# Performance work log

Hardware: AMD Instinct MI355X
Metric: run time of the kernel (lower is better)

## Reference

```python
import jax, jax.numpy as jnp
import numpy as np

B, S, D, H, HD, K, FF, G, E = 2, 2048, 512, 8, 64, 31, 2048, 4, 2
EPS = 1e-6


def _layer_norm(x, scale, bias):
    m = jnp.mean(x, axis=-1, keepdims=True)
    v = jnp.var(x, axis=-1, keepdims=True)
    return (x - m) * jax.lax.rsqrt(v + EPS) * scale + bias


def _forward(x, group_ids, p):
    (ln1_s, ln1_b, ck, cb, ln2_s, ln2_b,
     wq, bq, wk, bk, wv, bv, wo, bo, w1, b1, w2, b2) = p
    # ---- conv sublayer: LN -> Conv1d(SAME) -> gelu -> residual ----
    r = x
    h = _layer_norm(x, ln1_s, ln1_b)
    h = jax.lax.conv_general_dilated(h, ck, (1,), 'SAME',
                                     dimension_numbers=('NWC', 'WIO', 'NWC')) + cb
    x = jax.nn.gelu(h) + r
    # ---- self-attention sublayer: LN -> MHA -> residual ----
    r = x
    h = _layer_norm(x, ln2_s, ln2_b)
    q = jnp.einsum('bsd,dhk->bshk', h, wq) + bq   # [B,S,H,HD]
    k = jnp.einsum('bsd,dhk->bshk', h, wk) + bk
    v = jnp.einsum('bsd,dhk->bshk', h, wv) + bv
    scale = jnp.asarray(1.0 / np.sqrt(HD), h.dtype)
    att = jax.nn.softmax(jnp.einsum('bqhk,bshk->bhqs', q, k) * scale, axis=-1)
    o = jnp.einsum('bhqs,bshk->bqhk', att, v)
    x = jnp.einsum('bqhk,hkd->bqd', o, wo) + bo + r
    # ---- MoE sublayer: group tokens -> per-group experts -> mean -> combine ----
    r = x
    xf = x.reshape(-1, D)            # [N, D]
    gid = group_ids.reshape(-1)      # [N]
    # Each token routed by group_id gets the mean over that group's E experts.
    hid = jax.nn.gelu(jnp.einsum('nd,gedf->genf', xf, w1) + b1[:, :, None, :])  # [G,E,N,FF]
    ye = jnp.einsum('genf,gefd->gend', hid, w2) + b2[:, :, None, :]             # [G,E,N,D]
    yg = ye.mean(axis=1)                                                        # [G,N,D]
    sel = yg[gid, jnp.arange(gid.shape[0])]                                     # [N,D] combine by group id
    return sel.reshape(B, S, D) + r


def setup_inputs() -> dict:
    key = jax.random.key(0)
    ks = jax.random.split(key, 12)
    std = 0.02
    f32 = jnp.float32
    return {
        'x': jax.random.normal(ks[0], (B, S, D), f32),
        'group_ids': jax.random.randint(ks[1], (B, S), 0, G, jnp.int32),
        'ln1_scale': jnp.ones((D,), f32), 'ln1_bias': jnp.zeros((D,), f32),
        'conv_kernel': jax.random.normal(ks[2], (K, D, D), f32) * std,
        'conv_bias': jnp.zeros((D,), f32),
        'ln2_scale': jnp.ones((D,), f32), 'ln2_bias': jnp.zeros((D,), f32),
        'wq': jax.random.normal(ks[3], (D, H, HD), f32) * std, 'bq': jnp.zeros((H, HD), f32),
        'wk': jax.random.normal(ks[4], (D, H, HD), f32) * std, 'bk': jnp.zeros((H, HD), f32),
        'wv': jax.random.normal(ks[5], (D, H, HD), f32) * std, 'bv': jnp.zeros((H, HD), f32),
        'wo': jax.random.normal(ks[6], (H, HD, D), f32) * std, 'bo': jnp.zeros((D,), f32),
        'w1': jax.random.normal(ks[7], (G, E, D, FF), f32) * std, 'b1': jnp.zeros((G, E, FF), f32),
        'w2': jax.random.normal(ks[8], (G, E, FF, D), f32) * std, 'b2': jnp.zeros((G, E, D), f32),
    }


def reference(x, group_ids, ln1_scale, ln1_bias, conv_kernel, conv_bias,
              ln2_scale, ln2_bias, wq, bq, wk, bk, wv, bv, wo, bo,
              w1, b1, w2, b2):
    p = (ln1_scale, ln1_bias, conv_kernel, conv_bias, ln2_scale, ln2_bias,
         wq, bq, wk, bk, wv, bv, wo, bo, w1, b1, w2, b2)
    return _forward(x, group_ids, p)
```

## Files before the change

### kernel.cpp

```cpp
#include <hip/hip_runtime.h>
#include <hip/hip_bf16.h>
#include <math.h>
#include <stdint.h>

namespace {

constexpr int B_ = 2, S_ = 2048, D_ = 512, H_ = 8, HD_ = 64, K_ = 31,
              FF_ = 2048, G_ = 4, E_ = 2;
constexpr int N_ = B_ * S_;
constexpr int SP_ = S_ + 30;
constexpr float EPS_ = 1e-6f;
constexpr int PADCAP_ = 4608;

typedef __bf16 bf16x8 __attribute__((ext_vector_type(8)));
typedef unsigned short u16x8 __attribute__((ext_vector_type(8)));
typedef unsigned short u16x4 __attribute__((ext_vector_type(4)));
typedef float f32x4 __attribute__((ext_vector_type(4)));

__device__ __forceinline__ uint16_t f2bf(float f) {
  union { float f; uint32_t u; } v; v.f = f;
  uint32_t r = v.u + 0x7FFFu + ((v.u >> 16) & 1u);
  return (uint16_t)(r >> 16);
}
__device__ __forceinline__ float bf2f(uint16_t u) {
  union { uint32_t u; float f; } v; v.u = (uint32_t)u << 16;
  return v.f;
}

__device__ __forceinline__ float gelu_f(float x) {
  const float c = 0.7978845608028654f;
  return 0.5f * x * (1.0f + tanhf(c * (x + 0.044715f * x * x * x)));
}

#define GLOAD_LDS16(gsrc, ldst)                                              \
  __builtin_amdgcn_global_load_lds(                                          \
      (const __attribute__((address_space(1))) void*)(gsrc),                 \
      (__attribute__((address_space(3))) void*)(ldst), 16, 0, 0)

#define VMCNT(n) asm volatile("s_waitcnt vmcnt(" #n ")" ::: "memory")
#define MEMBAR asm volatile("" ::: "memory")
#define BARRIER __builtin_amdgcn_s_barrier()
#define PRIO1 __builtin_amdgcn_s_setprio(1)
#define PRIO0 __builtin_amdgcn_s_setprio(0)

__device__ __forceinline__ void kstep_swz(const char* As, const char* Bs,
                                          int wr, int wc, int l15, int g,
                                          f32x4 acc[4][4]) {
#pragma unroll
  for (int ks = 0; ks < 2; ++ks) {
    int co = (((ks << 2) | g) ^ (l15 & 7)) << 4;
    bf16x8 a[4], b[4];
#pragma unroll
    for (int m = 0; m < 4; ++m)
      a[m] = *(const bf16x8*)(As + (wr * 64 + m * 16 + l15) * 128 + co);
#pragma unroll
    for (int n = 0; n < 4; ++n)
      b[n] = *(const bf16x8*)(Bs + (wc * 64 + n * 16 + l15) * 128 + co);
    PRIO1;
#pragma unroll
    for (int m = 0; m < 4; ++m)
#pragma unroll
      for (int n = 0; n < 4; ++n)
        acc[m][n] = __builtin_amdgcn_mfma_f32_16x16x32_bf16(a[m], b[n], acc[m][n], 0, 0, 0);
    PRIO0;
  }
}

template <int NK>
__device__ __forceinline__ void gemm_k_dbuf64(const uint16_t* Ab, int lda,
                                              const uint16_t* Bb, int ldb,
                                              int t, int wr, int wc, int l15, int g,
                                              uint16_t (*As)[8192], uint16_t (*Bs)[8192],
                                              f32x4 acc[4][4]) {
  int r8 = t >> 3, clog = (t & 7) ^ (r8 & 7);
  int ubase = (t & ~63) * 8;
  auto stage = [&](int k0, int buf) {
#pragma unroll
    for (int pi = 0; pi < 4; ++pi) {
      int row = pi * 32 + r8;
      GLOAD_LDS16(Ab + (size_t)row * lda + k0 + clog * 8, As[buf] + pi * 2048 + ubase);
      GLOAD_LDS16(Bb + (size_t)row * ldb + k0 + clog * 8, Bs[buf] + pi * 2048 + ubase);
    }
  };
  stage(0, 0);
  int cur = 0;
  for (int ki = 0; ki < NK; ++ki) {
    if (ki + 1 < NK) {
      stage((ki + 1) * 64, cur ^ 1);
      VMCNT(8);
    } else {
      VMCNT(0);
    }
    BARRIER; MEMBAR;
    kstep_swz((const char*)As[cur], (const char*)Bs[cur], wr, wc, l15, g, acc);
    MEMBAR; BARRIER;
    cur ^= 1;
  }
}

__global__ __launch_bounds__(256) void prep_kernel(
    const float* __restrict__ ck, const float* __restrict__ wq,
    const float* __restrict__ wk, const float* __restrict__ wv,
    const float* __restrict__ wo, const float* __restrict__ w1,
    const float* __restrict__ w2, uint16_t* __restrict__ ckT,
    uint16_t* __restrict__ wqkvT, uint16_t* __restrict__ woT,
    uint16_t* __restrict__ w1T, uint16_t* __restrict__ w2T,
    uint16_t* __restrict__ Hpad, uint16_t* __restrict__ x2bf,
    const float* __restrict__ x, const float* __restrict__ ln1s,
    const float* __restrict__ ln1b, const int* __restrict__ gid,
    int* __restrict__ list, int* __restrict__ poff) {
  int bi = blockIdx.x, t = threadIdx.x;
  if (bi >= 25406) {
    int row = bi - 25406;
    const float* xr = x + (size_t)row * D_;
    float v0 = xr[t], v1 = xr[t + 256];
    float s = v0 + v1, sq = v0 * v0 + v1 * v1;
    for (int o = 32; o > 0; o >>= 1) {
      s += __shfl_down(s, o);
      sq += __shfl_down(sq, o);
    }
    __shared__ float sm[8];
    __shared__ float mr[2];
    int lane = t & 63, wid = t >> 6;
    if (lane == 0) { sm[wid] = s; sm[wid + 4] = sq; }
    __syncthreads();
    if (t == 0) {
      float ts = sm[0] + sm[1] + sm[2] + sm[3];
      float tq = sm[4] + sm[5] + sm[6] + sm[7];
      float m = ts / D_;
      mr[0] = m;
      mr[1] = rsqrtf(tq / D_ - m * m + EPS_);
    }
    __syncthreads();
    float m = mr[0], rs = mr[1];
    size_t drow = (size_t)(row >> 11) * SP_ + 15 + (row & 2047);
    uint16_t* orow = Hpad + drow * D_;
    orow[t] = f2bf((v0 - m) * rs * ln1s[t] + ln1b[t]);
    orow[t + 256] = f2bf((v1 - m) * rs * ln1s[t + 256] + ln1b[t + 256]);
    return;
  }
  if (bi == 25405) {
    __shared__ int cnt[G_], cur[G_];
    if (t < G_) cnt[t] = 0;
    __syncthreads();
    for (int i = t; i < N_; i += 256) atomicAdd(&cnt[gid[i]], 1);
    __syncthreads();
    if (t == 0) {
      int off = 0;
      for (int g = 0; g < G_; ++g) {
        poff[g] = off;
        cur[g] = off;
        off += (cnt[g] + 127) & ~127;
      }
      poff[G_] = off;
    }
    __syncthreads();
    for (int i = t; i < PADCAP_; i += 256) list[i] = N_;
    __syncthreads();
    for (int i = t; i < N_; i += 256) {
      int p = atomicAdd(&cur[gid[i]], 1);
      list[p] = i;
    }
    return;
  }
  if (bi >= 25344) {
    int j4 = bi - 25344;
    uint16_t* dst;
    if (j4 < 60) {
      int b = j4 / 30, j = j4 % 30;
      int row = b * SP_ + (j < 15 ? j : 2048 + j);
      dst = Hpad + (size_t)row * D_;
    } else {
      dst = x2bf + (size_t)N_ * D_;
    }
    dst[t] = 0;
    dst[t + 256] = 0;
    return;
  }
  const float* src;
  uint16_t* dst;
  int R, C, r0, c0;
  if (bi < 7936) {
    int z = bi >> 8, tile = bi & 255;
    R = 512; C = 512;
    c0 = (tile & 15) * 32; r0 = (tile >> 4) * 32;
    src = ck + (size_t)z * 262144; dst = ckT + (size_t)z * 262144;
  } else if (bi < 8960) {
    int idx = bi - 7936, mat = idx >> 8, tile = idx & 255;
    R = 512; C = 512;
    c0 = (tile & 15) * 32; r0 = (tile >> 4) * 32;
    src = mat == 0 ? wq : (mat == 1 ? wk : (mat == 2 ? wv : wo));
    dst = mat == 3 ? woT : wqkvT + (size_t)mat * 262144;
  } else if (bi < 17152) {
    int idx = bi - 8960, z = idx >> 10, tile = idx & 1023;
    R = 512; C = 2048;
    c0 = (tile & 63) * 32; r0 = (tile >> 6) * 32;
    src = w1 + (size_t)z * 1048576; dst = w1T + (size_t)z * 1048576;
  } else {
    int idx = bi - 17152, z = idx >> 10, tile = idx & 1023;
    R = 2048; C = 512;
    c0 = (tile & 15) * 32; r0 = (tile >> 4) * 32;
    src = w2 + (size_t)z * 1048576; dst = w2T + (size_t)z * 1048576;
  }
  __shared__ float tile[32][33];
  int tc = t & 31, tr = t >> 5;
#pragma unroll
  for (int i = 0; i < 4; ++i) {
    int r = tr + i * 8;
    tile[r][tc] = src[(size_t)(r0 + r) * C + c0 + tc];
  }
  __syncthreads();
#pragma unroll
  for (int i = 0; i < 4; ++i) {
    int rr = tr + i * 8;
    dst[(size_t)(c0 + rr) * R + r0 + tc] = f2bf(tile[tc][rr]);
  }
}

__global__ __launch_bounds__(512) void conv_mfma_kernel(
    const uint16_t* __restrict__ Hpad, const uint16_t* __restrict__ ckT,
    uint16_t* __restrict__ Pout) {
  __shared__ __align__(16) uint16_t As[2][20480];
  __shared__ __align__(16) uint16_t Bs[2][16384];
  int bid = blockIdx.x;
  int ks = bid & 7, tmn = bid >> 3, tm = tmn & 15, tn = tmn >> 4;
  int t = threadIdx.x;
  int w = t >> 6, l = t & 63, l15 = l & 15, g = l >> 4;
  int wr = w >> 2, wc = w & 3;
  int row0 = tm * 256, b = row0 >> 11, s0 = row0 & 2047;
  int kb = ks * 4, ntap = (ks == 7) ? 3 : 4;
  const uint16_t* Abase = Hpad + (size_t)(b * SP_ + s0 + kb) * D_;
  int r8 = t >> 3, clog = (t & 7) ^ (r8 & 7);
  int ubase = (t & ~63) * 8;
  f32x4 acc[8][4] = {};

  auto stageA = [&](int d0, int buf) {
#pragma unroll
    for (int pi = 0; pi < 5; ++pi)
      GLOAD_LDS16(Abase + (size_t)(pi * 64 + r8) * D_ + d0 + clog * 8,
                  As[buf] + pi * 4096 + ubase);
  };
  auto stageB = [&](int k, int d0, int buf) {
    const uint16_t* Bk = ckT + (size_t)k * D_ * D_ + (size_t)(tn * 256) * D_;
#pragma unroll
    for (int pi = 0; pi < 4; ++pi)
      GLOAD_LDS16(Bk + (size_t)(pi * 64 + r8) * D_ + d0 + clog * 8,
                  Bs[buf] + pi * 4096 + ubase);
  };

  stageA(0, 0);
  stageB(kb, 0, 0);
  int acur = 0, bcur = 0;
  for (int di = 0; di < 8; ++di) {
    int d0 = di * 64;
    for (int i = 0; i < ntap; ++i) {
      if (i + 1 < ntap) {
        stageB(kb + i + 1, d0, bcur ^ 1);
        VMCNT(4);
      } else if (di + 1 < 8) {
        stageA(d0 + 64, acur ^ 1);
        stageB(kb, d0 + 64, bcur ^ 1);
        VMCNT(9);
      } else {
        VMCNT(0);
      }
      BARRIER; MEMBAR;
      const char* Ac = (const char*)As[acur];
      const char* Bc = (const char*)Bs[bcur];
#pragma unroll
      for (int kk = 0; kk < 2; ++kk) {
        int cA = (((kk << 2) | g) ^ ((i + l15) & 7)) << 4;
        int cB = (((kk << 2) | g) ^ (l15 & 7)) << 4;
        bf16x8 a[8], bb[4];
#pragma unroll
        for (int m = 0; m < 8; ++m)
          a[m] = *(const bf16x8*)(Ac + (i + wr * 128 + m * 16 + l15) * 128 + cA);
#pragma unroll
        for (int n = 0; n < 4; ++n)
          bb[n] = *(const bf16x8*)(Bc + (wc * 64 + n * 16 + l15) * 128 + cB);
        PRIO1;
#pragma unroll
        for (int m = 0; m < 8; ++m)
#pragma unroll
          for (int n = 0; n < 4; ++n)
            acc[m][n] = __builtin_amdgcn_mfma_f32_16x16x32_bf16(a[m], bb[n], acc[m][n], 0, 0, 0);
        PRIO0;
      }
      MEMBAR; BARRIER;
      bcur ^= 1;
    }
    acur ^= 1;
  }
  uint16_t* P = Pout + (size_t)ks * N_ * D_;
#pragma unroll
  for (int m = 0; m < 8; ++m) {
    int r = row0 + wr * 128 + m * 16 + g * 4;
#pragma unroll
    for (int n = 0; n < 4; ++n) {
      int c = tn * 256 + wc * 64 + n * 16 + l15;
#pragma unroll
      for (int j = 0; j < 4; ++j)
        P[(size_t)(r + j) * D_ + c] = f2bf(acc[m][n][j]);
    }
  }
}

__global__ __launch_bounds__(256) void epi_ln_kernel(
    const uint16_t* __restrict__ P, const float* __restrict__ cb,
    const float* __restrict__ xres, const float* __restrict__ ln2s,
    const float* __restrict__ ln2b, float* __restrict__ x1,
    uint16_t* __restrict__ ln2bf) {
  int t = threadIdx.x;
  int row = blockIdx.x * 4 + (t >> 6);
  int l = t & 63, d0 = l * 8;
  size_t base = (size_t)row * D_ + d0;
  float v[8] = {};
#pragma unroll
  for (int q = 0; q < 8; ++q) {
    u16x8 pv = *(const u16x8*)(P + (size_t)q * N_ * D_ + base);
#pragma unroll
    for (int j = 0; j < 8; ++j) v[j] += bf2f(pv[j]);
  }
  float s = 0.f, sq = 0.f;
#pragma unroll
  for (int j = 0; j < 8; ++j) {
    float xv = xres[base + j];
    float vv = gelu_f(v[j] + cb[d0 + j]) + xv;
    v[j] = vv;
    s += vv;
    sq += vv * vv;
  }
  float4 o0 = {v[0], v[1], v[2], v[3]};
  float4 o1 = {v[4], v[5], v[6], v[7]};
  *(float4*)(x1 + base) = o0;
  *(float4*)(x1 + base + 4) = o1;
  for (int o = 1; o < 64; o <<= 1) {
    s += __shfl_xor(s, o);
    sq += __shfl_xor(sq, o);
  }
  float m = s / D_;
  float rs = rsqrtf(sq / D_ - m * m + EPS_);
  u16x8 ob;
#pragma unroll
  for (int j = 0; j < 8; ++j)
    ob[j] = f2bf((v[j] - m) * rs * ln2s[d0 + j] + ln2b[d0 + j]);
  *(u16x8*)(ln2bf + base) = ob;
}

__global__ __launch_bounds__(256) void gemm_qkv_kernel(
    const uint16_t* __restrict__ A, const uint16_t* __restrict__ BT,
    const float* __restrict__ bq, const float* __restrict__ bk,
    const float* __restrict__ bv, uint16_t* __restrict__ Qb,
    uint16_t* __restrict__ Kb, uint16_t* __restrict__ VT) {
  __shared__ __align__(16) uint16_t As[2][8192], Bs[2][8192];
  int tm = blockIdx.x, tn = blockIdx.y;
  int t = threadIdx.x;
  int w = t >> 6, l = t & 63, l15 = l & 15, g = l >> 4;
  int wr = w >> 1, wc = w & 1;
  int row0 = tm * 128;
  f32x4 acc[4][4] = {};
  gemm_k_dbuf64<8>(A + (size_t)row0 * D_, D_, BT + (size_t)(tn * 128) * D_, D_,
                   t, wr, wc, l15, g, As, Bs, acc);
  int sel = tn >> 2, col0 = (tn & 3) * 128;
  if (sel < 2) {
    uint16_t* dst = sel == 0 ? Qb : Kb;
    const float* bias = sel == 0 ? bq : bk;
    float scl = sel == 0 ? 0.18033688f : 1.0f;
#pragma unroll
    for (int m = 0; m < 4; ++m) {
      int r = row0 + wr * 64 + m * 16 + g * 4;
#pragma unroll
      for (int n = 0; n < 4; ++n) {
        int c = col0 + wc * 64 + n * 16 + l15;
#pragma unroll
        for (int j = 0; j < 4; ++j)
          dst[(size_t)(r + j) * D_ + c] = f2bf((acc[m][n][j] + bias[c]) * scl);
      }
    }
  } else {
#pragma unroll
    for (int m = 0; m < 4; ++m) {
      int tb = row0 + wr * 64 + m * 16 + g * 4;
      int b = tb >> 11, s = tb & 2047;
#pragma unroll
      for (int n = 0; n < 4; ++n) {
        int c = col0 + wc * 64 + n * 16 + l15;
        int hh = c >> 6, d = c & 63;
        u16x4 pack;
#pragma unroll
        for (int j = 0; j < 4; ++j) pack[j] = f2bf(acc[m][n][j] + bv[c]);
        *(u16x4*)(VT + ((size_t)((b * H_ + hh) * HD_ + d) * S_ + s)) = pack;
      }
    }
  }
}

__global__ __launch_bounds__(256) void gemm_wo_kernel(
    const uint16_t* __restrict__ A, const uint16_t* __restrict__ BT,
    const float* __restrict__ bo, const float* __restrict__ res,
    float* __restrict__ out, uint16_t* __restrict__ x2bf) {
  __shared__ __align__(16) uint16_t As[2][8192], Bs[2][8192];
  int tm = blockIdx.x, tn = blockIdx.y;
  int t = threadIdx.x;
  int w = t >> 6, l = t & 63, l15 = l & 15, g = l >> 4;
  int wr = w >> 1, wc = w & 1;
  int row0 = tm * 128;
  f32x4 acc[4][4] = {};
  gemm_k_dbuf64<8>(A + (size_t)row0 * D_, D_, BT + (size_t)(tn * 128) * D_, D_,
                   t, wr, wc, l15, g, As, Bs, acc);
#pragma unroll
  for (int m = 0; m < 4; ++m) {
    int r = row0 + wr * 64 + m * 16 + g * 4;
#pragma unroll
    for (int n = 0; n < 4; ++n) {
      int c = tn * 128 + wc * 64 + n * 16 + l15;
#pragma unroll
      for (int j = 0; j < 4; ++j) {
        float v = acc[m][n][j] + bo[c] + res[(size_t)(r + j) * D_ + c];
        out[(size_t)(r + j) * D_ + c] = v;
        x2bf[(size_t)(r + j) * D_ + c] = f2bf(v);
      }
    }
  }
}

__global__ __launch_bounds__(512) void attn_mfma_kernel(
    const uint16_t* __restrict__ Qbf, const uint16_t* __restrict__ Kbf,
    const uint16_t* __restrict__ VT, uint16_t* __restrict__ obf) {
  __shared__ __align__(16) uint16_t Ks[2][8192];
  __shared__ __align__(16) uint16_t Vt[2][8192];
  __shared__ __align__(16) uint16_t Plds[16384];
  int bid = blockIdx.x;
  int swz = (bid & 7) * 32 + (bid >> 3);
  int qt = swz & 15, h = (swz >> 4) & 7, b = swz >> 7;
  int t = threadIdx.x, w = t >> 6, l = t & 63;
  int l15 = l & 15, g = l >> 4;
  int qbase = b * S_ + qt * 128;
  bf16x8 qb_[2];
  {
    const uint16_t* qp = Qbf + (size_t)(qbase + w * 16 + l15) * D_ + h * HD_;
#pragma unroll
    for (int ks = 0; ks < 2; ++ks)
      qb_[ks] = *(const bf16x8*)(qp + ks * 32 + g * 8);
  }
  const uint16_t* Kbase = Kbf + (size_t)(b * S_) * D_ + h * HD_;
  const uint16_t* Vbase = VT + (size_t)((b * H_ + h) * HD_) * S_;
  int rk0 = t >> 3, rk1 = 64 + (t >> 3), pk = t & 7;
  int rv0 = t >> 4, rv1 = 32 + (t >> 4), pv = t & 15;
  int ck0 = (pk ^ (rk0 & 7)) << 4, ck1 = (pk ^ (rk1 & 7)) << 4;
  int cv0 = (pv ^ (rv0 & 7)) << 4, cv1 = (pv ^ (rv1 & 7)) << 4;
  int ldst0 = (t & ~63) << 4, ldst1 = (512 + (t & ~63)) << 4;

  auto stage_kv = [&](int kt, int buf) {
    const uint16_t* Kp = Kbase + (size_t)(kt * 128) * D_;
    const uint16_t* Vp = Vbase + kt * 128;
    GLOAD_LDS16((const char*)(Kp + (size_t)rk0 * D_) + ck0, (char*)Ks[buf] + ldst0);
    GLOAD_LDS16((const char*)(Kp + (size_t)rk1 * D_) + ck1, (char*)Ks[buf] + ldst1);
    GLOAD_LDS16((const char*)(Vp + (size_t)rv0 * S_) + cv0, (char*)Vt[buf] + ldst0);
    GLOAD_LDS16((const char*)(Vp + (size_t)rv1 * S_) + cv1, (char*)Vt[buf] + ldst1);
  };

  f32x4 acc_o[4] = {};
  float m_run = -INFINITY, l_run = 0.f;
  char* Pw = (char*)Plds + w * 4096;
  int swl = (l15 & 7) << 4;

  stage_kv(0, 0);
  int cur = 0;
  for (int kt = 0; kt < S_ / 128; ++kt) {
    if (kt + 1 < S_ / 128) {
      stage_kv(kt + 1, cur ^ 1);
      VMCNT(4);
    } else {
      VMCNT(0);
    }
    BARRIER; MEMBAR;
    const char* KsC = (const char*)Ks[cur];
    const char* VtC = (const char*)Vt[cur];
    f32x4 accs[8] = {};
#pragma unroll
    for (int ks = 0; ks < 2; ++ks) {
#pragma unroll
      for (int m = 0; m < 8; ++m) {
        int row = m * 16 + l15;
        bf16x8 kf = *(const bf16x8*)(KsC +
                        (row * 128 + ((ks * 64 + g * 16) ^ ((row & 7) << 4))));
        PRIO1;
        accs[m] = __builtin_amdgcn_mfma_f32_16x16x32_bf16(kf, qb_[ks], accs[m], 0, 0, 0);
        PRIO0;
      }
    }
    float mx = accs[0][0];
#pragma unroll
    for (int m = 0; m < 8; ++m)
#pragma unroll
      for (int j = 0; j < 4; ++j) mx = fmaxf(mx, accs[m][j]);
    mx = fmaxf(mx, __shfl_xor(mx, 16));
    mx = fmaxf(mx, __shfl_xor(mx, 32));
    if (!__all(mx <= m_run + 8.f)) {
      float mnew = fmaxf(m_run, mx);
      float corr = exp2f(m_run - mnew);
      m_run = mnew;
      l_run *= corr;
      float cj[4];
#pragma unroll
      for (int j = 0; j < 4; ++j) cj[j] = __shfl(corr, g * 4 + j);
#pragma unroll
      for (int n = 0; n < 4; ++n)
#pragma unroll
        for (int j = 0; j < 4; ++j) acc_o[n][j] *= cj[j];
    }
    float sum = 0.f;
#pragma unroll
    for (int m = 0; m < 8; ++m) {
      float p0 = exp2f(accs[m][0] - m_run);
      float p1 = exp2f(accs[m][1] - m_run);
      float p2 = exp2f(accs[m][2] - m_run);
      float p3 = exp2f(accs[m][3] - m_run);
      sum += (p0 + p1) + (p2 + p3);
      uint2 pk2;
      pk2.x = (uint32_t)f2bf(p0) | ((uint32_t)f2bf(p1) << 16);
      pk2.y = (uint32_t)f2bf(p2) | ((uint32_t)f2bf(p3) << 16);
      *(uint2*)(Pw + (l15 * 256 + ((m * 32 + g * 8) ^ swl))) = pk2;
    }
    sum += __shfl_xor(sum, 16);
    sum += __shfl_xor(sum, 32);
    l_run += sum;
#pragma unroll
    for (int s = 0; s < 4; ++s) {
      bf16x8 pa = *(const bf16x8*)(Pw + (l15 * 256 + ((s * 64 + g * 16) ^ swl)));
#pragma unroll
      for (int n = 0; n < 4; ++n) {
        int d = n * 16 + l15;
        bf16x8 vb = *(const bf16x8*)(VtC +
                        (d * 256 + ((s * 64 + g * 16) ^ ((d & 7) << 4))));
        PRIO1;
        acc_o[n] = __builtin_amdgcn_mfma_f32_16x16x32_bf16(pa, vb, acc_o[n], 0, 0, 0);
        PRIO0;
      }
    }
    MEMBAR; BARRIER;
    cur ^= 1;
  }
#pragma unroll
  for (int j = 0; j < 4; ++j) {
    float lr = __shfl(l_run, g * 4 + j);
    float inv = 1.f / lr;
    uint16_t* op = obf + (size_t)(qbase + w * 16 + g * 4 + j) * D_ + h * HD_;
#pragma unroll
    for (int n = 0; n < 4; ++n)
      op[n * 16 + l15] = f2bf(acc_o[n][j] * inv);
  }
}

__global__ __launch_bounds__(256) void ff1_mfma_kernel(
    const uint16_t* __restrict__ X, const uint16_t* __restrict__ w1T,
    const float* __restrict__ b1, const int* __restrict__ list,
    const int* __restrict__ poff, uint16_t* __restrict__ hid) {
  __shared__ __align__(16) uint16_t As[2][8192], Bs[2][8192];
  int tm = blockIdx.x, tn = blockIdx.y, e = blockIdx.z;
  int slot0 = tm * 128;
  if (slot0 >= poff[G_]) return;
  int g_ = 0;
#pragma unroll
  for (int gg = 1; gg < G_; ++gg) g_ += (slot0 >= poff[gg]);
  int t = threadIdx.x;
  int w = t >> 6, l = t & 63, l15 = l & 15, g = l >> 4;
  int wr = w >> 1, wc = w & 1;
  int r8 = t >> 3, clog = (t & 7) ^ (r8 & 7);
  int ubase = (t & ~63) * 8;
  int tok[4];
#pragma unroll
  for (int pi = 0; pi < 4; ++pi) tok[pi] = list[slot0 + pi * 32 + r8];
  const uint16_t* Bb = w1T + ((size_t)(g_ * E_ + e) * FF_ + tn * 128) * D_;
  f32x4 acc[4][4] = {};
  auto stage = [&](int k0, int buf) {
#pragma unroll
    for (int pi = 0; pi < 4; ++pi) {
      GLOAD_LDS16(X + (size_t)tok[pi] * D_ + k0 + clog * 8, As[buf] + pi * 2048 + ubase);
      GLOAD_LDS16(Bb + (size_t)(pi * 32 + r8) * D_ + k0 + clog * 8,
                  Bs[buf] + pi * 2048 + ubase);
    }
  };
  stage(0, 0);
  int cur = 0;
  for (int ki = 0; ki < 8; ++ki) {
    if (ki + 1 < 8) {
      stage((ki + 1) * 64, cur ^ 1);
      VMCNT(8);
    } else {
      VMCNT(0);
    }
    BARRIER; MEMBAR;
    kstep_swz((const char*)As[cur], (const char*)Bs[cur], wr, wc, l15, g, acc);
    MEMBAR; BARRIER;
    cur ^= 1;
  }
  const float* bias = b1 + (size_t)(g_ * E_ + e) * FF_;
  uint16_t* hidE = hid + (size_t)e * PADCAP_ * FF_;
#pragma unroll
  for (int m = 0; m < 4; ++m) {
    int r = slot0 + wr * 64 + m * 16 + g * 4;
#pragma unroll
    for (int n = 0; n < 4; ++n) {
      int c = tn * 128 + wc * 64 + n * 16 + l15;
#pragma unroll
      for (int j = 0; j < 4; ++j)
        hidE[(size_t)(r + j) * FF_ + c] = f2bf(gelu_f(acc[m][n][j] + bias[c]));
    }
  }
}

__global__ __launch_bounds__(256) void ff2_mfma_kernel(
    const uint16_t* __restrict__ hid, const uint16_t* __restrict__ w2T,
    const float* __restrict__ b2, const int* __restrict__ list,
    const int* __restrict__ poff, float* __restrict__ out) {
  __shared__ __align__(16) uint16_t As[2][4096];
  __shared__ __align__(16) uint16_t Bs[2][8192];
  int tm = blockIdx.x, tn = blockIdx.y, e = blockIdx.z;
  int slot0 = tm * 64;
  if (slot0 >= poff[G_]) return;
  int g_ = 0;
#pragma unroll
  for (int gg = 1; gg < G_; ++gg) g_ += (slot0 >= poff[gg]);
  int t = threadIdx.x;
  int w = t >> 6, l = t & 63, l15 = l & 15, g = l >> 4;
  int wr = w >> 1, wc = w & 1;
  int r8 = t >> 3, clog = (t & 7) ^ (r8 & 7);
  int ubase = (t & ~63) * 8;
  const uint16_t* Ab = hid + ((size_t)e * PADCAP_ + slot0) * FF_;
  const uint16_t* Bb = w2T + (size_t)(g_ * E_ + e) * D_ * FF_ + (size_t)(tn * 128) * FF_;
  f32x4 acc[2][4] = {};
  auto stage = [&](int k0, int buf) {
#pragma unroll
    for (int pi = 0; pi < 2; ++pi)
      GLOAD_LDS16(Ab + (size_t)(pi * 32 + r8) * FF_ + k0 + clog * 8,
                  As[buf] + pi * 2048 + ubase);
#pragma unroll
    for (int pi = 0; pi < 4; ++pi)
      GLOAD_LDS16(Bb + (size_t)(pi * 32 + r8) * FF_ + k0 + clog * 8,
                  Bs[buf] + pi * 2048 + ubase);
  };
  stage(0, 0);
  int cur = 0;
  for (int ki = 0; ki < 32; ++ki) {
    if (ki + 1 < 32) {
      stage((ki + 1) * 64, cur ^ 1);
      VMCNT(6);
    } else {
      VMCNT(0);
    }
    BARRIER; MEMBAR;
    const char* Ac = (const char*)As[cur];
    const char* Bc = (const char*)Bs[cur];
#pragma unroll
    for (int ks = 0; ks < 2; ++ks) {
      int co = (((ks << 2) | g) ^ (l15 & 7)) << 4;
      bf16x8 a[2], b[4];
#pragma unroll
      for (int m = 0; m < 2; ++m)
        a[m] = *(const bf16x8*)(Ac + (wr * 32 + m * 16 + l15) * 128 + co);
#pragma unroll
      for (int n = 0; n < 4; ++n)
        b[n] = *(const bf16x8*)(Bc + (wc * 64 + n * 16 + l15) * 128 + co);
      PRIO1;
#pragma unroll
      for (int m = 0; m < 2; ++m)
#pragma unroll
        for (int n = 0; n < 4; ++n)
          acc[m][n] = __builtin_amdgcn_mfma_f32_16x16x32_bf16(a[m], b[n], acc[m][n], 0, 0, 0);
      PRIO0;
    }
    MEMBAR; BARRIER;
    cur ^= 1;
  }
  const float* be = b2 + (size_t)(g_ * E_ + e) * D_;
#pragma unroll
  for (int m = 0; m < 2; ++m) {
    int rbase = slot0 + wr * 32 + m * 16 + g * 4;
#pragma unroll
    for (int j = 0; j < 4; ++j) {
      int tok = list[rbase + j];
      if (tok >= N_) continue;
#pragma unroll
      for (int n = 0; n < 4; ++n) {
        int c = tn * 128 + wc * 64 + n * 16 + l15;
        atomicAdd(&out[(size_t)tok * D_ + c], 0.5f * (acc[m][n][j] + be[c]));
      }
    }
  }
}

}

extern "C" void kernel_launch(void* const* d_in, const int* in_sizes, int n_in,
                              void* d_out, int out_size, void* d_ws, size_t ws_size,
                              hipStream_t stream) {
  const float* x = (const float*)d_in[0];
  const int* gid = (const int*)d_in[1];
  const float* ln1s = (const float*)d_in[2];
  const float* ln1b = (const float*)d_in[3];
  const float* ck = (const float*)d_in[4];
  const float* cb = (const float*)d_in[5];
  const float* ln2s = (const float*)d_in[6];
  const float* ln2b = (const float*)d_in[7];
  const float* wq = (const float*)d_in[8];
  const float* bq = (const float*)d_in[9];
  const float* wk = (const float*)d_in[10];
  const float* bk = (const float*)d_in[11];
  const float* wv = (const float*)d_in[12];
  const float* bv = (const float*)d_in[13];
  const float* wo = (const float*)d_in[14];
  const float* bo = (const float*)d_in[15];
  const float* w1 = (const float*)d_in[16];
  const float* b1 = (const float*)d_in[17];
  const float* w2 = (const float*)d_in[18];
  const float* b2 = (const float*)d_in[19];
  float* out = (float*)d_out;

  char* ws = (char*)d_ws;
  char* A = ws;
  uint16_t* P = (uint16_t*)A;
  uint16_t* ln2bf = (uint16_t*)(A + (32ull << 20));
  uint16_t* Qbf = (uint16_t*)A;
  uint16_t* Kbf = (uint16_t*)(A + (4ull << 20));
  uint16_t* VT = (uint16_t*)(A + (8ull << 20));
  uint16_t* obf = (uint16_t*)(A + (12ull << 20));
  uint16_t* hidbf = (uint16_t*)A;

  float* x1 = (float*)(ws + (38ull << 20));
  uint16_t* Hpad = (uint16_t*)(ws + (46ull << 20));
  uint16_t* ckT = (uint16_t*)(ws + (51ull << 20));
  uint16_t* wqkvT = (uint16_t*)(ws + (67ull << 20));
  uint16_t* woT = (uint16_t*)(ws + (69ull << 20));
  uint16_t* w1T = (uint16_t*)(ws + (70ull << 20));
  uint16_t* w2T = (uint16_t*)(ws + (86ull << 20));
  uint16_t* x2bf = (uint16_t*)(ws + (102ull << 20));
  int* list = (int*)(ws + (107ull << 20));
  int* poff = list + PADCAP_;

  prep_kernel<<<29502, 256, 0, stream>>>(ck, wq, wk, wv, wo, w1, w2,
                                         ckT, wqkvT, woT, w1T, w2T, Hpad, x2bf,
                                         x, ln1s, ln1b, gid, list, poff);

  conv_mfma_kernel<<<256, 512, 0, stream>>>(Hpad, ckT, P);
  epi_ln_kernel<<<1024, 256, 0, stream>>>(P, cb, x, ln2s, ln2b, x1, ln2bf);

  gemm_qkv_kernel<<<dim3(32, 12), 256, 0, stream>>>(ln2bf, wqkvT, bq, bk, bv, Qbf, Kbf, VT);
  attn_mfma_kernel<<<256, 512, 0, stream>>>(Qbf, Kbf, VT, obf);
  gemm_wo_kernel<<<dim3(32, 4), 256, 0, stream>>>(obf, woT, bo, x1, out, x2bf);

  ff1_mfma_kernel<<<dim3(36, 16, 2), 256, 0, stream>>>(x2bf, w1T, b1, list, poff, hidbf);
  ff2_mfma_kernel<<<dim3(72, 4, 2), 256, 0, stream>>>(hidbf, w2T, b2, list, poff, out);
}
```

Before: 289.3 us.

## Interleave LDS reads with MFMA in conv loop and enlarge FF1 tiles to 256x256

The conv kernel's inner tap loop now splits LDS fragment reads into quarters and interleaves them with MFMA groups under extra barriers. The next stage's global-to-LDS loads are issued after the first fragment read, and the vmcnt wait is deferred to the last quarter, so loads overlap more compute. FF1 moves to 512-thread blocks with 256x256 tiles, and group padding is raised to 256 rows, with PADCAP and workspace offsets grown to match. The aim is more data reuse per block and fewer blocks, at the cost of more padding waste, doubled LDS use and lower occupancy.

```diff
diff --git a/kernel.cpp b/kernel.cpp
--- a/kernel.cpp
+++ b/kernel.cpp
@@ -10,7 +10,7 @@
 constexpr int N_ = B_ * S_;
 constexpr int SP_ = S_ + 30;
 constexpr float EPS_ = 1e-6f;
-constexpr int PADCAP_ = 4608;
+constexpr int PADCAP_ = 5120;
 
 typedef __bf16 bf16x8 __attribute__((ext_vector_type(8)));
 typedef unsigned short u16x8 __attribute__((ext_vector_type(8)));
@@ -150,7 +150,7 @@
       for (int g = 0; g < G_; ++g) {
         poff[g] = off;
         cur[g] = off;
-        off += (cnt[g] + 127) & ~127;
+        off += (cnt[g] + 255) & ~255;
       }
       poff[G_] = off;
     }
@@ -250,42 +250,64 @@
 
   stageA(0, 0);
   stageB(kb, 0, 0);
+  VMCNT(0);
+  BARRIER; MEMBAR;
+
   int acur = 0, bcur = 0;
   for (int di = 0; di < 8; ++di) {
     int d0 = di * 64;
     for (int i = 0; i < ntap; ++i) {
+      const char* Ac = (const char*)As[acur];
+      const char* Bc = (const char*)Bs[bcur];
+      bf16x8 a[4], bb[4];
+      auto rdA = [&](int kkq, int mh) {
+        int cA = (((kkq << 2) | g) ^ ((i + l15) & 7)) << 4;
+#pragma unroll
+        for (int mi = 0; mi < 4; ++mi)
+          a[mi] = *(const bf16x8*)(Ac + (i + wr * 128 + (mh * 4 + mi) * 16 + l15) * 128 + cA);
+      };
+      auto rdB = [&](int kkq) {
+        int cB = (((kkq << 2) | g) ^ (l15 & 7)) << 4;
+#pragma unroll
+        for (int n = 0; n < 4; ++n)
+          bb[n] = *(const bf16x8*)(Bc + (wc * 64 + n * 16 + l15) * 128 + cB);
+      };
+      auto mma = [&](int mh) {
+        PRIO1;
+#pragma unroll
+        for (int mi = 0; mi < 4; ++mi)
+#pragma unroll
+          for (int n = 0; n < 4; ++n)
+            acc[mh * 4 + mi][n] = __builtin_amdgcn_mfma_f32_16x16x32_bf16(
+                a[mi], bb[n], acc[mh * 4 + mi][n], 0, 0, 0);
+        PRIO0;
+      };
+      rdA(0, 0); rdB(0);
+      MEMBAR;
       if (i + 1 < ntap) {
         stageB(kb + i + 1, d0, bcur ^ 1);
-        VMCNT(4);
       } else if (di + 1 < 8) {
         stageA(d0 + 64, acur ^ 1);
         stageB(kb, d0 + 64, bcur ^ 1);
-        VMCNT(9);
-      } else {
-        VMCNT(0);
       }
-      BARRIER; MEMBAR;
-      const char* Ac = (const char*)As[acur];
-      const char* Bc = (const char*)Bs[bcur];
-#pragma unroll
-      for (int kk = 0; kk < 2; ++kk) {
-        int cA = (((kk << 2) | g) ^ ((i + l15) & 7)) << 4;
-        int cB = (((kk << 2) | g) ^ (l15 & 7)) << 4;
-        bf16x8 a[8], bb[4];
-#pragma unroll
-        for (int m = 0; m < 8; ++m)
-          a[m] = *(const bf16x8*)(Ac + (i + wr * 128 + m * 16 + l15) * 128 + cA);
-#pragma unroll
-        for (int n = 0; n < 4; ++n)
-          bb[n] = *(const bf16x8*)(Bc + (wc * 64 + n * 16 + l15) * 128 + cB);
-        PRIO1;
-#pragma unroll
-        for (int m = 0; m < 8; ++m)
-#pragma unroll
-          for (int n = 0; n < 4; ++n)
-            acc[m][n] = __builtin_amdgcn_mfma_f32_16x16x32_bf16(a[m], bb[n], acc[m][n], 0, 0, 0);
-        PRIO0;
-      }
+      BARRIER;
+      mma(0);
+      MEMBAR; BARRIER;
+      rdA(0, 1);
+      MEMBAR;
+      BARRIER;
+      mma(1);
+      MEMBAR; BARRIER;
+      rdA(1, 0); rdB(1);
+      MEMBAR;
+      BARRIER;
+      mma(0);
+      MEMBAR; BARRIER;
+      rdA(1, 1);
+      MEMBAR;
+      VMCNT(0);
+      BARRIER;
+      mma(1);
       MEMBAR; BARRIER;
       bcur ^= 1;
     }
@@ -553,33 +575,33 @@
   }
 }
 
-__global__ __launch_bounds__(256) void ff1_mfma_kernel(
+__global__ __launch_bounds__(512) void ff1_mfma_kernel(
     const uint16_t* __restrict__ X, const uint16_t* __restrict__ w1T,
     const float* __restrict__ b1, const int* __restrict__ list,
     const int* __restrict__ poff, uint16_t* __restrict__ hid) {
-  __shared__ __align__(16) uint16_t As[2][8192], Bs[2][8192];
+  __shared__ __align__(16) uint16_t As[2][16384], Bs[2][16384];
   int tm = blockIdx.x, tn = blockIdx.y, e = blockIdx.z;
-  int slot0 = tm * 128;
+  int slot0 = tm * 256;
   if (slot0 >= poff[G_]) return;
   int g_ = 0;
 #pragma unroll
   for (int gg = 1; gg < G_; ++gg) g_ += (slot0 >= poff[gg]);
   int t = threadIdx.x;
   int w = t >> 6, l = t & 63, l15 = l & 15, g = l >> 4;
-  int wr = w >> 1, wc = w & 1;
+  int wr = w >> 2, wc = w & 3;
   int r8 = t >> 3, clog = (t & 7) ^ (r8 & 7);
   int ubase = (t & ~63) * 8;
   int tok[4];
 #pragma unroll
-  for (int pi = 0; pi < 4; ++pi) tok[pi] = list[slot0 + pi * 32 + r8];
-  const uint16_t* Bb = w1T + ((size_t)(g_ * E_ + e) * FF_ + tn * 128) * D_;
-  f32x4 acc[4][4] = {};
+  for (int pi = 0; pi < 4; ++pi) tok[pi] = list[slot0 + pi * 64 + r8];
+  const uint16_t* Bb = w1T + ((size_t)(g_ * E_ + e) * FF_ + tn * 256) * D_;
+  f32x4 acc[8][4] = {};
   auto stage = [&](int k0, int buf) {
 #pragma unroll
     for (int pi = 0; pi < 4; ++pi) {
-      GLOAD_LDS16(X + (size_t)tok[pi] * D_ + k0 + clog * 8, As[buf] + pi * 2048 + ubase);
-      GLOAD_LDS16(Bb + (size_t)(pi * 32 + r8) * D_ + k0 + clog * 8,
-                  Bs[buf] + pi * 2048 + ubase);
+      GLOAD_LDS16(X + (size_t)tok[pi] * D_ + k0 + clog * 8, As[buf] + pi * 4096 + ubase);
+      GLOAD_LDS16(Bb + (size_t)(pi * 64 + r8) * D_ + k0 + clog * 8,
+                  Bs[buf] + pi * 4096 + ubase);
     }
   };
   stage(0, 0);
@@ -592,18 +614,37 @@
       VMCNT(0);
     }
     BARRIER; MEMBAR;
-    kstep_swz((const char*)As[cur], (const char*)Bs[cur], wr, wc, l15, g, acc);
+    const char* Ac = (const char*)As[cur];
+    const char* Bc = (const char*)Bs[cur];
+#pragma unroll
+    for (int kk = 0; kk < 2; ++kk) {
+      int co = (((kk << 2) | g) ^ (l15 & 7)) << 4;
+      bf16x8 a[8], bb[4];
+#pragma unroll
+      for (int m = 0; m < 8; ++m)
+        a[m] = *(const bf16x8*)(Ac + (wr * 128 + m * 16 + l15) * 128 + co);
+#pragma unroll
+      for (int n = 0; n < 4; ++n)
+        bb[n] = *(const bf16x8*)(Bc + (wc * 64 + n * 16 + l15) * 128 + co);
+      PRIO1;
+#pragma unroll
+      for (int m = 0; m < 8; ++m)
+#pragma unroll
+        for (int n = 0; n < 4; ++n)
+          acc[m][n] = __builtin_amdgcn_mfma_f32_16x16x32_bf16(a[m], bb[n], acc[m][n], 0, 0, 0);
+      PRIO0;
+    }
     MEMBAR; BARRIER;
     cur ^= 1;
   }
   const float* bias = b1 + (size_t)(g_ * E_ + e) * FF_;
   uint16_t* hidE = hid + (size_t)e * PADCAP_ * FF_;
 #pragma unroll
-  for (int m = 0; m < 4; ++m) {
-    int r = slot0 + wr * 64 + m * 16 + g * 4;
+  for (int m = 0; m < 8; ++m) {
+    int r = slot0 + wr * 128 + m * 16 + g * 4;
 #pragma unroll
     for (int n = 0; n < 4; ++n) {
-      int c = tn * 128 + wc * 64 + n * 16 + l15;
+      int c = tn * 256 + wc * 64 + n * 16 + l15;
 #pragma unroll
       for (int j = 0; j < 4; ++j)
         hidE[(size_t)(r + j) * FF_ + c] = f2bf(gelu_f(acc[m][n][j] + bias[c]));
@@ -728,15 +769,15 @@
   uint16_t* obf = (uint16_t*)(A + (12ull << 20));
   uint16_t* hidbf = (uint16_t*)A;
 
-  float* x1 = (float*)(ws + (38ull << 20));
-  uint16_t* Hpad = (uint16_t*)(ws + (46ull << 20));
-  uint16_t* ckT = (uint16_t*)(ws + (51ull << 20));
-  uint16_t* wqkvT = (uint16_t*)(ws + (67ull << 20));
-  uint16_t* woT = (uint16_t*)(ws + (69ull << 20));
-  uint16_t* w1T = (uint16_t*)(ws + (70ull << 20));
-  uint16_t* w2T = (uint16_t*)(ws + (86ull << 20));
-  uint16_t* x2bf = (uint16_t*)(ws + (102ull << 20));
-  int* list = (int*)(ws + (107ull << 20));
+  float* x1 = (float*)(ws + (40ull << 20));
+  uint16_t* Hpad = (uint16_t*)(ws + (48ull << 20));
+  uint16_t* ckT = (uint16_t*)(ws + (53ull << 20));
+  uint16_t* wqkvT = (uint16_t*)(ws + (69ull << 20));
+  uint16_t* woT = (uint16_t*)(ws + (72ull << 20));
+  uint16_t* w1T = (uint16_t*)(ws + (73ull << 20));
+  uint16_t* w2T = (uint16_t*)(ws + (89ull << 20));
+  uint16_t* x2bf = (uint16_t*)(ws + (105ull << 20));
+  int* list = (int*)(ws + (110ull << 20));
   int* poff = list + PADCAP_;
 
   prep_kernel<<<29502, 256, 0, stream>>>(ck, wq, wk, wv, wo, w1, w2,
@@ -750,6 +791,6 @@
   attn_mfma_kernel<<<256, 512, 0, stream>>>(Qbf, Kbf, VT, obf);
   gemm_wo_kernel<<<dim3(32, 4), 256, 0, stream>>>(obf, woT, bo, x1, out, x2bf);
 
-  ff1_mfma_kernel<<<dim3(36, 16, 2), 256, 0, stream>>>(x2bf, w1T, b1, list, poff, hidbf);
-  ff2_mfma_kernel<<<dim3(72, 4, 2), 256, 0, stream>>>(hidbf, w2T, b2, list, poff, out);
-}
+  ff1_mfma_kernel<<<dim3(20, 8, 2), 512, 0, stream>>>(x2bf, w1T, b1, list, poff, hidbf);
+  ff2_mfma_kernel<<<dim3(80, 4, 2), 256, 0, stream>>>(hidbf, w2T, b2, list, poff, out);
+}
```

New measurement: 300.9 us. +4.0%, slower.

## Restructure conv GEMM inner loop into interleaved LDS-read/MFMA phases with barriers

Applied to the files above, without the earlier changes.

Splits each tap iteration of the conv implicit GEMM into four phases, each reading half the A fragments (and B when needed) from LDS and then issuing 16 MFMAs, with barriers between phases. The next global-to-LDS prefetch is issued after the first LDS reads, and the wait for it moves to the end of the tap instead of before compute. The aim is to overlap global loads with MFMA work and to cut register pressure from holding 8 A fragments at once. In exchange it adds several workgroup barriers per tap, which can serialize waves.

```diff
diff --git a/kernel.cpp b/kernel.cpp
--- a/kernel.cpp
+++ b/kernel.cpp
@@ -250,42 +250,64 @@
 
   stageA(0, 0);
   stageB(kb, 0, 0);
+  VMCNT(0);
+  BARRIER; MEMBAR;
+
   int acur = 0, bcur = 0;
   for (int di = 0; di < 8; ++di) {
     int d0 = di * 64;
     for (int i = 0; i < ntap; ++i) {
+      const char* Ac = (const char*)As[acur];
+      const char* Bc = (const char*)Bs[bcur];
+      bf16x8 a[4], bb[4];
+      auto rdA = [&](int kkq, int mh) {
+        int cA = (((kkq << 2) | g) ^ ((i + l15) & 7)) << 4;
+#pragma unroll
+        for (int mi = 0; mi < 4; ++mi)
+          a[mi] = *(const bf16x8*)(Ac + (i + wr * 128 + (mh * 4 + mi) * 16 + l15) * 128 + cA);
+      };
+      auto rdB = [&](int kkq) {
+        int cB = (((kkq << 2) | g) ^ (l15 & 7)) << 4;
+#pragma unroll
+        for (int n = 0; n < 4; ++n)
+          bb[n] = *(const bf16x8*)(Bc + (wc * 64 + n * 16 + l15) * 128 + cB);
+      };
+      auto mma = [&](int mh) {
+        PRIO1;
+#pragma unroll
+        for (int mi = 0; mi < 4; ++mi)
+#pragma unroll
+          for (int n = 0; n < 4; ++n)
+            acc[mh * 4 + mi][n] = __builtin_amdgcn_mfma_f32_16x16x32_bf16(
+                a[mi], bb[n], acc[mh * 4 + mi][n], 0, 0, 0);
+        PRIO0;
+      };
+      rdA(0, 0); rdB(0);
+      MEMBAR;
       if (i + 1 < ntap) {
         stageB(kb + i + 1, d0, bcur ^ 1);
-        VMCNT(4);
       } else if (di + 1 < 8) {
         stageA(d0 + 64, acur ^ 1);
         stageB(kb, d0 + 64, bcur ^ 1);
-        VMCNT(9);
-      } else {
-        VMCNT(0);
       }
-      BARRIER; MEMBAR;
-      const char* Ac = (const char*)As[acur];
-      const char* Bc = (const char*)Bs[bcur];
-#pragma unroll
-      for (int kk = 0; kk < 2; ++kk) {
-        int cA = (((kk << 2) | g) ^ ((i + l15) & 7)) << 4;
-        int cB = (((kk << 2) | g) ^ (l15 & 7)) << 4;
-        bf16x8 a[8], bb[4];
-#pragma unroll
-        for (int m = 0; m < 8; ++m)
-          a[m] = *(const bf16x8*)(Ac + (i + wr * 128 + m * 16 + l15) * 128 + cA);
-#pragma unroll
-        for (int n = 0; n < 4; ++n)
-          bb[n] = *(const bf16x8*)(Bc + (wc * 64 + n * 16 + l15) * 128 + cB);
-        PRIO1;
-#pragma unroll
-        for (int m = 0; m < 8; ++m)
-#pragma unroll
-          for (int n = 0; n < 4; ++n)
-            acc[m][n] = __builtin_amdgcn_mfma_f32_16x16x32_bf16(a[m], bb[n], acc[m][n], 0, 0, 0);
-        PRIO0;
-      }
+      BARRIER;
+      mma(0);
+      MEMBAR; BARRIER;
+      rdA(0, 1);
+      MEMBAR;
+      BARRIER;
+      mma(1);
+      MEMBAR; BARRIER;
+      rdA(1, 0); rdB(1);
+      MEMBAR;
+      BARRIER;
+      mma(0);
+      MEMBAR; BARRIER;
+      rdA(1, 1);
+      MEMBAR;
+      VMCNT(0);
+      BARRIER;
+      mma(1);
       MEMBAR; BARRIER;
       bcur ^= 1;
     }
```

Result: no change. 287.2 us (median of 3 runs) (-0.7%).

## Use one barrier per k-step in double-buffered GEMM and attention loops

Applied to the files above, without the earlier changes.

Every double-buffered loop (generic GEMM, conv, attention, FF1, FF2) now has a single barrier per iteration. The barrier sits at the top, the next tile's prefetch is issued after it, and each wave waits on its own loads (vmcnt 0) at the end of the iteration. This drops the trailing barrier that guarded buffer reuse and is meant to cut synchronisation stalls. The catch is that the prefetch now overlaps only the current compute rather than being issued a full step ahead, and the full vmcnt drain may expose load latency.

```diff
diff --git a/kernel.cpp b/kernel.cpp
--- a/kernel.cpp
+++ b/kernel.cpp
@@ -83,17 +83,14 @@
     }
   };
   stage(0, 0);
+  VMCNT(0);
   int cur = 0;
   for (int ki = 0; ki < NK; ++ki) {
-    if (ki + 1 < NK) {
-      stage((ki + 1) * 64, cur ^ 1);
-      VMCNT(8);
-    } else {
-      VMCNT(0);
-    }
     BARRIER; MEMBAR;
+    if (ki + 1 < NK) stage((ki + 1) * 64, cur ^ 1);
     kstep_swz((const char*)As[cur], (const char*)Bs[cur], wr, wc, l15, g, acc);
-    MEMBAR; BARRIER;
+    MEMBAR;
+    VMCNT(0);
     cur ^= 1;
   }
 }
@@ -250,21 +247,19 @@
 
   stageA(0, 0);
   stageB(kb, 0, 0);
+  VMCNT(0);
+
   int acur = 0, bcur = 0;
   for (int di = 0; di < 8; ++di) {
     int d0 = di * 64;
     for (int i = 0; i < ntap; ++i) {
+      BARRIER; MEMBAR;
       if (i + 1 < ntap) {
         stageB(kb + i + 1, d0, bcur ^ 1);
-        VMCNT(4);
       } else if (di + 1 < 8) {
         stageA(d0 + 64, acur ^ 1);
         stageB(kb, d0 + 64, bcur ^ 1);
-        VMCNT(9);
-      } else {
-        VMCNT(0);
-      }
-      BARRIER; MEMBAR;
+      }
       const char* Ac = (const char*)As[acur];
       const char* Bc = (const char*)Bs[bcur];
 #pragma unroll
@@ -286,7 +281,8 @@
             acc[m][n] = __builtin_amdgcn_mfma_f32_16x16x32_bf16(a[m], bb[n], acc[m][n], 0, 0, 0);
         PRIO0;
       }
-      MEMBAR; BARRIER;
+      MEMBAR;
+      VMCNT(0);
       bcur ^= 1;
     }
     acur ^= 1;
@@ -466,15 +462,11 @@
   int swl = (l15 & 7) << 4;
 
   stage_kv(0, 0);
+  VMCNT(0);
   int cur = 0;
   for (int kt = 0; kt < S_ / 128; ++kt) {
-    if (kt + 1 < S_ / 128) {
-      stage_kv(kt + 1, cur ^ 1);
-      VMCNT(4);
-    } else {
-      VMCNT(0);
-    }
     BARRIER; MEMBAR;
+    if (kt + 1 < S_ / 128) stage_kv(kt + 1, cur ^ 1);
     const char* KsC = (const char*)Ks[cur];
     const char* VtC = (const char*)Vt[cur];
     f32x4 accs[8] = {};
@@ -539,7 +531,8 @@
         PRIO0;
       }
     }
-    MEMBAR; BARRIER;
+    MEMBAR;
+    VMCNT(0);
     cur ^= 1;
   }
 #pragma unroll
@@ -583,17 +576,14 @@
     }
   };
   stage(0, 0);
+  VMCNT(0);
   int cur = 0;
   for (int ki = 0; ki < 8; ++ki) {
-    if (ki + 1 < 8) {
-      stage((ki + 1) * 64, cur ^ 1);
-      VMCNT(8);
-    } else {
-      VMCNT(0);
-    }
     BARRIER; MEMBAR;
+    if (ki + 1 < 8) stage((ki + 1) * 64, cur ^ 1);
     kstep_swz((const char*)As[cur], (const char*)Bs[cur], wr, wc, l15, g, acc);
-    MEMBAR; BARRIER;
+    MEMBAR;
+    VMCNT(0);
     cur ^= 1;
   }
   const float* bias = b1 + (size_t)(g_ * E_ + e) * FF_;
@@ -642,15 +632,11 @@
                   Bs[buf] + pi * 2048 + ubase);
   };
   stage(0, 0);
+  VMCNT(0);
   int cur = 0;
   for (int ki = 0; ki < 32; ++ki) {
-    if (ki + 1 < 32) {
-      stage((ki + 1) * 64, cur ^ 1);
-      VMCNT(6);
-    } else {
-      VMCNT(0);
-    }
     BARRIER; MEMBAR;
+    if (ki + 1 < 32) stage((ki + 1) * 64, cur ^ 1);
     const char* Ac = (const char*)As[cur];
     const char* Bc = (const char*)Bs[cur];
 #pragma unroll
@@ -671,7 +657,8 @@
           acc[m][n] = __builtin_amdgcn_mfma_f32_16x16x32_bf16(a[m], b[n], acc[m][n], 0, 0, 0);
       PRIO0;
     }
-    MEMBAR; BARRIER;
+    MEMBAR;
+    VMCNT(0);
     cur ^= 1;
   }
   const float* be = b2 + (size_t)(g_ * E_ + e) * D_;
```

Result: no change. 291.7 us (+0.8%).
